# Performance work log

Measured on AMD Instinct MI355X. Metric: run time of the kernel, lower is better.

## Reference

```python
import jax, jax.numpy as jnp
import numpy as np

NUM_HEADS = 16
NEG_BIG = -1.0e9


def setup_inputs() -> dict:
    key = jax.random.key(0)
    k1, k2, k3 = jax.random.split(key, 3)
    B, S, D = 2, 2048, 1024
    x = jax.random.normal(k1, (B, S, D), dtype=jnp.float32)
    qkv_weights = jax.random.normal(k2, (D, 3 * D), dtype=jnp.float32) * (1.0 / np.sqrt(D))
    output_weights = jax.random.normal(k3, (D, D), dtype=jnp.float32) * (1.0 / np.sqrt(D))
    return {"x": x, "qkv_weights": qkv_weights, "output_weights": output_weights}


def reference(x, qkv_weights, output_weights):
    B, S, D = x.shape
    H = NUM_HEADS
    hd = D // H
    qkv = jnp.einsum('bsd,de->bse', x, qkv_weights)  # [B,S,3D]
    q, k, v = jnp.split(qkv, 3, axis=-1)
    # [B,H,S,hd]
    q = q.reshape(B, S, H, hd).transpose(0, 2, 1, 3)
    k = k.reshape(B, S, H, hd).transpose(0, 2, 1, 3)
    v = v.reshape(B, S, H, hd).transpose(0, 2, 1, 3)
    scores = jnp.einsum('bhqd,bhkd->bhqk', q, k)  # unscaled, matches original masked path
    # original bug: when masked, softmax is applied to UNSCALED scores with mask
    tril = jnp.tril(jnp.ones((S, S), dtype=scores.dtype))
    masked = scores * tril + NEG_BIG * (1.0 - tril)
    attn = jax.nn.softmax(masked, axis=-1)
    heads = jnp.einsum('bhqk,bhkd->bhqd', attn, v)  # [B,H,S,hd]
    merged = heads.transpose(0, 2, 1, 3).reshape(B, S, D)
    return jnp.einsum('bsd,de->bse', merged, output_weights)
```

## Files before the change

### kernel.cpp

```cpp
#include <hip/hip_runtime.h>
#include <stdint.h>

using u16 = unsigned short;
typedef __attribute__((ext_vector_type(8))) _Float16 half8;
typedef __attribute__((ext_vector_type(4))) float f32x4;
typedef __attribute__((ext_vector_type(4))) unsigned short u16x4;

#define S_LEN 2048
#define D_MODEL 1024
#define NHEAD 16
#define HDIM 64

__device__ __forceinline__ u16 f2h_bits(float f){
    _Float16 h = (_Float16)f;
    return __builtin_bit_cast(u16, h);
}
__device__ __forceinline__ float h2f_bits(u16 v){
    return (float)__builtin_bit_cast(_Float16, v);
}

typedef __attribute__((address_space(1))) void gvoid;
typedef __attribute__((address_space(3))) void lvoid;
__device__ __forceinline__ void gload_lds16(const u16* g, u16* l){
    __builtin_amdgcn_global_load_lds((gvoid*)(uintptr_t)g, (lvoid*)l, 16, 0, 0);
}

__global__ __launch_bounds__(256) void k_cvt_x(const float* __restrict__ x, u16* __restrict__ xh){
    int i = blockIdx.x*256 + threadIdx.x;
    float4 v = reinterpret_cast<const float4*>(x)[i];
    u16x4 o;
    o.x = f2h_bits(v.x); o.y = f2h_bits(v.y); o.z = f2h_bits(v.z); o.w = f2h_bits(v.w);
    reinterpret_cast<u16x4*>(xh)[i] = o;
}

__global__ __launch_bounds__(256) void k_cvt_wT(const float* __restrict__ W, u16* __restrict__ WT,
                                                int K, int N){
    __shared__ float t[32][33];
    int tx = threadIdx.x & 31, ty = threadIdx.x >> 5;
    int n0 = blockIdx.x*32, k0 = blockIdx.y*32;
    #pragma unroll
    for (int i=0;i<4;++i) t[ty+8*i][tx] = W[(size_t)(k0+ty+8*i)*N + n0+tx];
    __syncthreads();
    #pragma unroll
    for (int i=0;i<4;++i) WT[(size_t)(n0+ty+8*i)*K + k0+tx] = f2h_bits(t[tx][ty+8*i]);
}

template<int EPI>
__global__ __launch_bounds__(256) void k_gemm(const u16* __restrict__ A, const u16* __restrict__ BT,
                                              float* __restrict__ Cf, u16* __restrict__ Qh,
                                              u16* __restrict__ Kh, u16* __restrict__ Vt){
    constexpr int Kd = 1024;
    __shared__ u16 As[128*32];
    __shared__ u16 Bs[128*32];
    int nwg = gridDim.x;
    int cpx = nwg >> 3;
    int wg  = ((int)blockIdx.x & 7)*cpx + ((int)blockIdx.x >> 3);
    int tm = wg & 31, tn = wg >> 5;
    int t = threadIdx.x;
    int w = t >> 6, lane = t & 63;
    int lr = lane & 15, lg = lane >> 4;
    int wm = (w>>1)*64, wn = (w&1)*64;
    int m0 = tm*128 + wm, n0 = tn*128 + wn;

    const u16* aG = A  + (size_t)(tm*128 + (t>>2))*Kd + (t&3)*8;
    const u16* bG = BT + (size_t)(tn*128 + (t>>2))*Kd + (t&3)*8;
    u16* aL = As + (t>>2)*32 + (t&3)*8;
    u16* bL = Bs + (t>>2)*32 + (t&3)*8;

    f32x4 acc[4][4];
    #pragma unroll
    for (int i=0;i<4;++i)
        #pragma unroll
        for (int j=0;j<4;++j) acc[i][j] = (f32x4){0.f,0.f,0.f,0.f};

    for (int kk=0; kk<Kd; kk+=32){
        gload_lds16(aG + kk, aL);
        gload_lds16(aG + kk + (size_t)64*Kd, aL + 64*32);
        gload_lds16(bG + kk, bL);
        gload_lds16(bG + kk + (size_t)64*Kd, bL + 64*32);
        __syncthreads();

        half8 av[4], bv[4];
        #pragma unroll
        for (int mf=0;mf<4;++mf) av[mf] = *reinterpret_cast<const half8*>(&As[(wm+mf*16+lr)*32 + lg*8]);
        #pragma unroll
        for (int nf=0;nf<4;++nf) bv[nf] = *reinterpret_cast<const half8*>(&Bs[(wn+nf*16+lr)*32 + lg*8]);
        __builtin_amdgcn_s_setprio(1);
        #pragma unroll
        for (int mf=0;mf<4;++mf)
            #pragma unroll
            for (int nf=0;nf<4;++nf)
                acc[mf][nf] = __builtin_amdgcn_mfma_f32_16x16x32_f16(av[mf], bv[nf], acc[mf][nf], 0,0,0);
        __builtin_amdgcn_s_setprio(0);
        __syncthreads();
    }

    if (EPI == 0){
        #pragma unroll
        for (int mf=0;mf<4;++mf)
            #pragma unroll
            for (int nf=0;nf<4;++nf)
                #pragma unroll
                for (int j=0;j<4;++j)
                    Cf[(size_t)(m0+mf*16+lg*4+j)*D_MODEL + n0+nf*16+lr] = acc[mf][nf][j];
    } else {
        #pragma unroll
        for (int mf=0;mf<4;++mf){
            int r0 = m0 + mf*16 + lg*4;
            int b  = r0 >> 11, s = r0 & 2047;
            #pragma unroll
            for (int nf=0;nf<4;++nf){
                int col = n0 + nf*16 + lr;
                int which = col >> 10;
                int d  = col & 1023;
                int h  = d >> 6, di = d & 63;
                int bh = b*NHEAD + h;
                if (which == 2){
                    u16x4 pv;
                    pv.x = f2h_bits(acc[mf][nf][0]);
                    pv.y = f2h_bits(acc[mf][nf][1]);
                    pv.z = f2h_bits(acc[mf][nf][2]);
                    pv.w = f2h_bits(acc[mf][nf][3]);
                    *reinterpret_cast<u16x4*>(Vt + ((size_t)bh*HDIM + di)*S_LEN + s) = pv;
                } else {
                    u16* dst = (which==0 ? Qh : Kh) + ((size_t)bh*S_LEN + s)*HDIM + di;
                    #pragma unroll
                    for (int j=0;j<4;++j) dst[(size_t)j*HDIM] = f2h_bits(acc[mf][nf][j]);
                }
            }
        }
    }
}

__global__ __launch_bounds__(256,3) void k_attn(const u16* __restrict__ Q, const u16* __restrict__ K,
                                                const u16* __restrict__ Vt, u16* __restrict__ Mg,
                                                u16* __restrict__ On, float* __restrict__ Ml,
                                                float* __restrict__ Ll){
    __shared__ u16 Kl[64*64];
    __shared__ u16 Vl[64*64];
    __shared__ u16 plds[4][32][72];
    int t = threadIdx.x;
    int w = t >> 6, lane = t & 63;
    int lr = lane & 15, lg = lane >> 4;
    int blk = blockIdx.x;
    int bh  = blk & 31;
    int p   = blk >> 5;
    int qb, ktLo, ktHi, part; bool split;
    if (p < 8)      { qb = p;    ktLo = 0;      ktHi = 2*p+2;   split = false; part = 0; }
    else if (p < 16){ qb = 23-p; ktLo = 0;      ktHi = qb+1;    split = true;  part = 0; }
    else            { qb = 31-p; ktLo = qb+1;   ktHi = 2*qb+2;  split = true;  part = 1; }
    int q0w = qb*128 + w*32;
    int b = bh >> 4, h = bh & 15;
    int pid = split ? ((bh<<3) + (qb-8))*2 + part : 0;
    const u16* Qp = Q  + (size_t)bh*S_LEN*HDIM;
    const u16* Kp = K  + (size_t)bh*S_LEN*HDIM;
    const u16* Vp = Vt + (size_t)bh*HDIM*S_LEN;

    int c0 = t, c1 = t + 256;
    int r0 = c0 >> 3, s0 = 8*((c0 & 7) ^ (r0 & 7));
    int r1 = c1 >> 3, s1 = 8*((c1 & 7) ^ (r1 & 7));
    const u16* Ks0 = Kp + (size_t)r0*HDIM + s0;
    const u16* Ks1 = Kp + (size_t)r1*HDIM + s1;
    const u16* Vs0 = Vp + (size_t)r0*S_LEN + s0;
    const u16* Vs1 = Vp + (size_t)r1*S_LEN + s1;
    u16* Kd0 = Kl + c0*8; u16* Kd1 = Kl + c1*8;
    u16* Vd0 = Vl + c0*8; u16* Vd1 = Vl + c1*8;

    half8 qf[2][2];
    #pragma unroll
    for (int qi=0;qi<2;++qi)
        #pragma unroll
        for (int ks=0;ks<2;++ks){
            half8 v = *reinterpret_cast<const half8*>(Qp + (size_t)(q0w+qi*16+lr)*HDIM + ks*32 + lg*8);
            #pragma unroll
            for (int j=0;j<8;++j) v[j] = v[j] * (_Float16)1.44269504f;
            qf[qi][ks] = v;
        }

    f32x4 oacc[2][4];
    float mrow[2], lrow[2];
    #pragma unroll
    for (int mf=0;mf<2;++mf){
        #pragma unroll
        for (int nf=0;nf<4;++nf) oacc[mf][nf] = (f32x4){0.f,0.f,0.f,0.f};
        mrow[mf] = -1e30f; lrow[mf] = 0.f;
    }

    int lastkt = (q0w + 31) >> 6;
    int swz = (lr & 7)*8;

    for (int kt=ktLo; kt<ktHi; ++kt){
        int kbase = kt*64;
        gload_lds16(Ks0 + (size_t)kbase*HDIM, Kd0);
        gload_lds16(Ks1 + (size_t)kbase*HDIM, Kd1);
        gload_lds16(Vs0 + kbase, Vd0);
        gload_lds16(Vs1 + kbase, Vd1);
        __syncthreads();

        if (kt <= lastkt){
            half8 kfr[4][2];
            #pragma unroll
            for (int kf=0;kf<4;++kf)
                #pragma unroll
                for (int ks=0;ks<2;++ks)
                    kfr[kf][ks] = *reinterpret_cast<const half8*>(Kl + (kf*16+lr)*64 + ((ks*32 + lg*8) ^ swz));
            f32x4 sc[4][2];
            #pragma unroll
            for (int kf=0;kf<4;++kf)
                #pragma unroll
                for (int qi=0;qi<2;++qi) sc[kf][qi] = (f32x4){0.f,0.f,0.f,0.f};
            __builtin_amdgcn_s_setprio(1);
            #pragma unroll
            for (int kf=0;kf<4;++kf)
                #pragma unroll
                for (int qi=0;qi<2;++qi)
                    #pragma unroll
                    for (int ks=0;ks<2;++ks)
                        sc[kf][qi] = __builtin_amdgcn_mfma_f32_16x16x32_f16(kfr[kf][ks], qf[qi][ks], sc[kf][qi], 0,0,0);
            __builtin_amdgcn_s_setprio(0);

            half8 vf[4][2];
            #pragma unroll
            for (int nf=0;nf<4;++nf)
                #pragma unroll
                for (int kh=0;kh<2;++kh)
                    vf[nf][kh] = *reinterpret_cast<const half8*>(Vl + (nf*16+lr)*64 + ((kh*32 + lg*8) ^ swz));

            if (kt == lastkt){
                #pragma unroll
                for (int kf=0;kf<4;++kf)
                    #pragma unroll
                    for (int qi=0;qi<2;++qi)
                        #pragma unroll
                        for (int j=0;j<4;++j)
                            if (kbase+kf*16+lg*4+j > q0w+qi*16+lr) sc[kf][qi][j] = -1e9f;
            }

            float pmax[2];
            #pragma unroll
            for (int qi=0;qi<2;++qi){
                float t0 = fmaxf(fmaxf(sc[0][qi][0], sc[0][qi][1]), fmaxf(sc[0][qi][2], sc[0][qi][3]));
                float t1 = fmaxf(fmaxf(sc[1][qi][0], sc[1][qi][1]), fmaxf(sc[1][qi][2], sc[1][qi][3]));
                float t2 = fmaxf(fmaxf(sc[2][qi][0], sc[2][qi][1]), fmaxf(sc[2][qi][2], sc[2][qi][3]));
                float t3 = fmaxf(fmaxf(sc[3][qi][0], sc[3][qi][1]), fmaxf(sc[3][qi][2], sc[3][qi][3]));
                float tm = fmaxf(fmaxf(t0,t1), fmaxf(t2,t3));
                tm = fmaxf(tm, __shfl_xor(tm,16));
                tm = fmaxf(tm, __shfl_xor(tm,32));
                pmax[qi] = tm;
            }
            bool need = (pmax[0] > mrow[0]+8.0f) || (pmax[1] > mrow[1]+8.0f);
            if (__any(need)){
                float aq[2];
                #pragma unroll
                for (int qi=0;qi<2;++qi){
                    float mnew = fmaxf(mrow[qi], pmax[qi]);
                    aq[qi] = __builtin_amdgcn_exp2f(mrow[qi] - mnew);
                    mrow[qi] = mnew;
                    lrow[qi] *= aq[qi];
                }
                float am[2][4];
                #pragma unroll
                for (int mf=0;mf<2;++mf)
                    #pragma unroll
                    for (int j=0;j<4;++j) am[mf][j] = __shfl(aq[mf], lg*4+j);
                #pragma unroll
                for (int mf=0;mf<2;++mf)
                    #pragma unroll
                    for (int nf=0;nf<4;++nf)
                        #pragma unroll
                        for (int j=0;j<4;++j) oacc[mf][nf][j] *= am[mf][j];
            }
            #pragma unroll
            for (int qi=0;qi<2;++qi){
                float m = mrow[qi];
                float rs = 0.f;
                #pragma unroll
                for (int kf=0;kf<4;++kf)
                    #pragma unroll
                    for (int j=0;j<4;++j){
                        float e = __builtin_amdgcn_exp2f(sc[kf][qi][j] - m);
                        sc[kf][qi][j] = e;
                        rs += e;
                    }
                rs += __shfl_xor(rs,16);
                rs += __shfl_xor(rs,32);
                lrow[qi] += rs;
            }
            #pragma unroll
            for (int kf=0;kf<4;++kf)
                #pragma unroll
                for (int qi=0;qi<2;++qi){
                    u16x4 pk;
                    pk.x = f2h_bits(sc[kf][qi][0]);
                    pk.y = f2h_bits(sc[kf][qi][1]);
                    pk.z = f2h_bits(sc[kf][qi][2]);
                    pk.w = f2h_bits(sc[kf][qi][3]);
                    *reinterpret_cast<u16x4*>(&plds[w][qi*16+lr][kf*16+lg*4]) = pk;
                }
            half8 pa[2][2];
            #pragma unroll
            for (int mf=0;mf<2;++mf)
                #pragma unroll
                for (int kh=0;kh<2;++kh)
                    pa[mf][kh] = *reinterpret_cast<const half8*>(&plds[w][mf*16+lr][kh*32 + lg*8]);
            __builtin_amdgcn_s_setprio(1);
            #pragma unroll
            for (int mf=0;mf<2;++mf)
                #pragma unroll
                for (int nf=0;nf<4;++nf)
                    #pragma unroll
                    for (int kh=0;kh<2;++kh)
                        oacc[mf][nf] = __builtin_amdgcn_mfma_f32_16x16x32_f16(pa[mf][kh], vf[nf][kh], oacc[mf][nf], 0,0,0);
            __builtin_amdgcn_s_setprio(0);
        }
        __syncthreads();
    }

    float linv[2][4];
    #pragma unroll
    for (int mf=0;mf<2;++mf)
        #pragma unroll
        for (int j=0;j<4;++j) linv[mf][j] = 1.0f/__shfl(lrow[mf], lg*4+j);
    if (!split){
        #pragma unroll
        for (int mf=0;mf<2;++mf)
            #pragma unroll
            for (int nf=0;nf<4;++nf)
                #pragma unroll
                for (int j=0;j<4;++j)
                    Mg[(size_t)(b*S_LEN + q0w + mf*16 + lg*4 + j)*D_MODEL + h*HDIM + nf*16 + lr]
                        = f2h_bits(oacc[mf][nf][j]*linv[mf][j]);
    } else {
        #pragma unroll
        for (int mf=0;mf<2;++mf)
            #pragma unroll
            for (int nf=0;nf<4;++nf)
                #pragma unroll
                for (int j=0;j<4;++j)
                    On[pid*8192 + (w*32 + mf*16 + lg*4 + j)*64 + nf*16 + lr]
                        = f2h_bits(oacc[mf][nf][j]*linv[mf][j]);
        if (lg == 0){
            #pragma unroll
            for (int qi=0;qi<2;++qi){
                Ml[pid*128 + w*32 + qi*16 + lr] = mrow[qi];
                Ll[pid*128 + w*32 + qi*16 + lr] = lrow[qi];
            }
        }
    }
}

__global__ __launch_bounds__(256) void k_comb(const u16* __restrict__ On, const float* __restrict__ Ml,
                                              const float* __restrict__ Ll, u16* __restrict__ Mg){
    int blk = blockIdx.x;
    int bh = blk & 31;
    int q8 = blk >> 5;
    int qb = 8 + q8;
    int b = bh >> 4, h = bh & 15;
    int t = threadIdx.x;
    int c = t & 63, rg = t >> 6;
    int pid0 = ((bh<<3) + q8)*2, pid1 = pid0 + 1;
    #pragma unroll 4
    for (int i=0;i<32;++i){
        int r = rg*32 + i;
        float m1 = Ml[pid0*128 + r], m2 = Ml[pid1*128 + r];
        float l1 = Ll[pid0*128 + r], l2 = Ll[pid1*128 + r];
        float M  = fmaxf(m1, m2);
        float w1 = l1*__builtin_amdgcn_exp2f(m1 - M);
        float w2 = l2*__builtin_amdgcn_exp2f(m2 - M);
        float o1 = h2f_bits(On[pid0*8192 + r*64 + c]);
        float o2 = h2f_bits(On[pid1*8192 + r*64 + c]);
        float o  = (w1*o1 + w2*o2) / (w1 + w2);
        Mg[(size_t)(b*S_LEN + qb*128 + r)*D_MODEL + h*HDIM + c] = f2h_bits(o);
    }
}

extern "C" void kernel_launch(void* const* d_in, const int* in_sizes, int n_in,
                              void* d_out, int out_size, void* d_ws, size_t ws_size,
                              hipStream_t stream) {
    const float* x    = (const float*)d_in[0];
    const float* wqkv = (const float*)d_in[1];
    const float* wout = (const float*)d_in[2];
    float* out = (float*)d_out;
    char* ws = (char*)d_ws;

    const size_t MB = 1u<<20;
    u16* xh     = (u16*)(ws + 0*MB);
    u16* wqkvT  = (u16*)(ws + 8*MB);
    u16* woutT  = (u16*)(ws + 14*MB);
    u16* Qh     = (u16*)(ws + 16*MB);
    u16* Kh     = (u16*)(ws + 24*MB);
    u16* Vt     = (u16*)(ws + 32*MB);
    u16* Mg     = (u16*)(ws + 40*MB);
    u16* On     = (u16*)(ws + 48*MB);
    float* Ml   = (float*)(ws + 56*MB);
    float* Ll   = (float*)(ws + 56*MB + 256*1024);

    k_cvt_x <<<4096, 256, 0, stream>>>(x, xh);
    k_cvt_wT<<<dim3(96,32), 256, 0, stream>>>(wqkv, wqkvT, 1024, 3072);
    k_cvt_wT<<<dim3(32,32), 256, 0, stream>>>(wout, woutT, 1024, 1024);
    k_gemm<1><<<768, 256, 0, stream>>>(xh, wqkvT, nullptr, Qh, Kh, Vt);
    k_attn  <<<768, 256, 0, stream>>>(Qh, Kh, Vt, Mg, On, Ml, Ll);
    k_comb  <<<256, 256, 0, stream>>>(On, Ml, Ll, Mg);
    k_gemm<0><<<256, 256, 0, stream>>>(Mg, woutT, out, nullptr, nullptr, nullptr);
}
```

Before: 129.5 us.

## Double-buffer LDS tiles in GEMM and attention, merge weight-convert launches

Adds two-stage LDS double buffering to both the GEMM and attention kernels. The next K or KV tile is prefetched with global_load_lds while the current tile is computed, and the leading barrier before compute is dropped. The two weight-transpose/convert launches are merged into one grid. The change doubles LDS use per block, which may lower occupancy, and the barrier ordering between the prefetch and reads of the other buffer has to stay correct.

```diff
diff --git a/kernel.cpp b/kernel.cpp
--- a/kernel.cpp
+++ b/kernel.cpp
@@ -33,16 +33,20 @@
     reinterpret_cast<u16x4*>(xh)[i] = o;
 }
 
-__global__ __launch_bounds__(256) void k_cvt_wT(const float* __restrict__ W, u16* __restrict__ WT,
-                                                int K, int N){
-    __shared__ float t[32][33];
+__global__ __launch_bounds__(256) void k_cvt_w(const float* __restrict__ W0, u16* __restrict__ T0,
+                                               const float* __restrict__ W1, u16* __restrict__ T1){
+    __shared__ float tt[32][33];
+    int bx = blockIdx.x;
+    const float* W; u16* WT; int N, n0;
+    if (bx < 96){ W = W0; WT = T0; N = 3072; n0 = bx*32; }
+    else        { W = W1; WT = T1; N = 1024; n0 = (bx-96)*32; }
+    int k0 = blockIdx.y*32;
     int tx = threadIdx.x & 31, ty = threadIdx.x >> 5;
-    int n0 = blockIdx.x*32, k0 = blockIdx.y*32;
-    #pragma unroll
-    for (int i=0;i<4;++i) t[ty+8*i][tx] = W[(size_t)(k0+ty+8*i)*N + n0+tx];
+    #pragma unroll
+    for (int i=0;i<4;++i) tt[ty+8*i][tx] = W[(size_t)(k0+ty+8*i)*N + n0+tx];
     __syncthreads();
     #pragma unroll
-    for (int i=0;i<4;++i) WT[(size_t)(n0+ty+8*i)*K + k0+tx] = f2h_bits(t[tx][ty+8*i]);
+    for (int i=0;i<4;++i) WT[(size_t)(n0+ty+8*i)*1024 + k0+tx] = f2h_bits(tt[tx][ty+8*i]);
 }
 
 template<int EPI>
@@ -50,8 +54,8 @@
                                               float* __restrict__ Cf, u16* __restrict__ Qh,
                                               u16* __restrict__ Kh, u16* __restrict__ Vt){
     constexpr int Kd = 1024;
-    __shared__ u16 As[128*32];
-    __shared__ u16 Bs[128*32];
+    __shared__ u16 As[2*128*32];
+    __shared__ u16 Bs[2*128*32];
     int nwg = gridDim.x;
     int cpx = nwg >> 3;
     int wg  = ((int)blockIdx.x & 7)*cpx + ((int)blockIdx.x >> 3);
@@ -67,24 +71,30 @@
     u16* aL = As + (t>>2)*32 + (t&3)*8;
     u16* bL = Bs + (t>>2)*32 + (t&3)*8;
 
+    auto stage = [&](int buf, int kk){
+        gload_lds16(aG + kk, aL + buf*4096);
+        gload_lds16(aG + kk + (size_t)64*Kd, aL + buf*4096 + 64*32);
+        gload_lds16(bG + kk, bL + buf*4096);
+        gload_lds16(bG + kk + (size_t)64*Kd, bL + buf*4096 + 64*32);
+    };
+
     f32x4 acc[4][4];
     #pragma unroll
     for (int i=0;i<4;++i)
         #pragma unroll
         for (int j=0;j<4;++j) acc[i][j] = (f32x4){0.f,0.f,0.f,0.f};
 
+    stage(0, 0);
+    __syncthreads();
     for (int kk=0; kk<Kd; kk+=32){
-        gload_lds16(aG + kk, aL);
-        gload_lds16(aG + kk + (size_t)64*Kd, aL + 64*32);
-        gload_lds16(bG + kk, bL);
-        gload_lds16(bG + kk + (size_t)64*Kd, bL + 64*32);
-        __syncthreads();
+        int cur = (kk>>5) & 1;
+        if (kk+32 < Kd) stage(cur^1, kk+32);
 
         half8 av[4], bv[4];
         #pragma unroll
-        for (int mf=0;mf<4;++mf) av[mf] = *reinterpret_cast<const half8*>(&As[(wm+mf*16+lr)*32 + lg*8]);
-        #pragma unroll
-        for (int nf=0;nf<4;++nf) bv[nf] = *reinterpret_cast<const half8*>(&Bs[(wn+nf*16+lr)*32 + lg*8]);
+        for (int mf=0;mf<4;++mf) av[mf] = *reinterpret_cast<const half8*>(&As[cur*4096 + (wm+mf*16+lr)*32 + lg*8]);
+        #pragma unroll
+        for (int nf=0;nf<4;++nf) bv[nf] = *reinterpret_cast<const half8*>(&Bs[cur*4096 + (wn+nf*16+lr)*32 + lg*8]);
         __builtin_amdgcn_s_setprio(1);
         #pragma unroll
         for (int mf=0;mf<4;++mf)
@@ -136,8 +146,8 @@
                                                 const u16* __restrict__ Vt, u16* __restrict__ Mg,
                                                 u16* __restrict__ On, float* __restrict__ Ml,
                                                 float* __restrict__ Ll){
-    __shared__ u16 Kl[64*64];
-    __shared__ u16 Vl[64*64];
+    __shared__ u16 Kl[2*64*64];
+    __shared__ u16 Vl[2*64*64];
     __shared__ u16 plds[4][32][72];
     int t = threadIdx.x;
     int w = t >> 6, lane = t & 63;
@@ -166,6 +176,14 @@
     u16* Kd0 = Kl + c0*8; u16* Kd1 = Kl + c1*8;
     u16* Vd0 = Vl + c0*8; u16* Vd1 = Vl + c1*8;
 
+    auto stageKV = [&](int buf, int kt){
+        int kbase = kt*64;
+        gload_lds16(Ks0 + (size_t)kbase*HDIM, Kd0 + buf*4096);
+        gload_lds16(Ks1 + (size_t)kbase*HDIM, Kd1 + buf*4096);
+        gload_lds16(Vs0 + kbase, Vd0 + buf*4096);
+        gload_lds16(Vs1 + kbase, Vd1 + buf*4096);
+    };
+
     half8 qf[2][2];
     #pragma unroll
     for (int qi=0;qi<2;++qi)
@@ -188,22 +206,25 @@
 
     int lastkt = (q0w + 31) >> 6;
     int swz = (lr & 7)*8;
-
-    for (int kt=ktLo; kt<ktHi; ++kt){
-        int kbase = kt*64;
-        gload_lds16(Ks0 + (size_t)kbase*HDIM, Kd0);
-        gload_lds16(Ks1 + (size_t)kbase*HDIM, Kd1);
-        gload_lds16(Vs0 + kbase, Vd0);
-        gload_lds16(Vs1 + kbase, Vd1);
-        __syncthreads();
+    int nT = ktHi - ktLo;
+
+    stageKV(0, ktLo);
+    __syncthreads();
+    for (int i=0; i<nT; ++i){
+        int kt = ktLo + i;
+        int cur = i & 1;
+        if (i+1 < nT) stageKV(cur^1, kt+1);
 
         if (kt <= lastkt){
+            const u16* Kb = Kl + cur*4096;
+            const u16* Vb = Vl + cur*4096;
+            int kbase = kt*64;
             half8 kfr[4][2];
             #pragma unroll
             for (int kf=0;kf<4;++kf)
                 #pragma unroll
                 for (int ks=0;ks<2;++ks)
-                    kfr[kf][ks] = *reinterpret_cast<const half8*>(Kl + (kf*16+lr)*64 + ((ks*32 + lg*8) ^ swz));
+                    kfr[kf][ks] = *reinterpret_cast<const half8*>(Kb + (kf*16+lr)*64 + ((ks*32 + lg*8) ^ swz));
             f32x4 sc[4][2];
             #pragma unroll
             for (int kf=0;kf<4;++kf)
@@ -224,7 +245,7 @@
             for (int nf=0;nf<4;++nf)
                 #pragma unroll
                 for (int kh=0;kh<2;++kh)
-                    vf[nf][kh] = *reinterpret_cast<const half8*>(Vl + (nf*16+lr)*64 + ((kh*32 + lg*8) ^ swz));
+                    vf[nf][kh] = *reinterpret_cast<const half8*>(Vb + (nf*16+lr)*64 + ((kh*32 + lg*8) ^ swz));
 
             if (kt == lastkt){
                 #pragma unroll
@@ -396,8 +417,7 @@
     float* Ll   = (float*)(ws + 56*MB + 256*1024);
 
     k_cvt_x <<<4096, 256, 0, stream>>>(x, xh);
-    k_cvt_wT<<<dim3(96,32), 256, 0, stream>>>(wqkv, wqkvT, 1024, 3072);
-    k_cvt_wT<<<dim3(32,32), 256, 0, stream>>>(wout, woutT, 1024, 1024);
+    k_cvt_w <<<dim3(128,32), 256, 0, stream>>>(wqkv, wqkvT, wout, woutT);
     k_gemm<1><<<768, 256, 0, stream>>>(xh, wqkvT, nullptr, Qh, Kh, Vt);
     k_attn  <<<768, 256, 0, stream>>>(Qh, Kh, Vt, Mg, On, Ml, Ll);
     k_comb  <<<256, 256, 0, stream>>>(On, Ml, Ll, Mg);
```

Measured after the change: 119.6 us. -7.6%, faster.
